# Kernel tuning notes

Measured on AMD Instinct MI355X. Metric: run time of the kernel, lower is better.

Reference implementation:

```python
import jax, jax.numpy as jnp
import numpy as np

BS, X_DIM, KEY_DIM, N_KEYS, TOPK = 16384, 4096, 512, 4096, 16


def setup_inputs() -> dict:
    key = jax.random.key(0)
    k_x, k_keys, k_w, k_b = jax.random.split(key, 4)
    bound = 1.0 / np.sqrt(X_DIM)  # torch Linear default init range
    return {
        "x": jax.random.normal(k_x, (BS, X_DIM), dtype=jnp.float32),
        "keys": jax.random.normal(k_keys, (N_KEYS, KEY_DIM), dtype=jnp.float32),
        "W": jax.random.uniform(k_w, (KEY_DIM, X_DIM), dtype=jnp.float32, minval=-bound, maxval=bound),
        "b": jax.random.uniform(k_b, (KEY_DIM,), dtype=jnp.float32, minval=-bound, maxval=bound),
        "topk": TOPK,
    }


def reference(x, keys, W, b, topk):
    # query = projection(x): [bs, key_dim]
    query = jnp.einsum("bx,kx->bk", x, W) + b
    # scores = query @ keys^T: [bs, n_keys]
    scores = jnp.einsum("bd,nd->bn", query, keys)
    real_topk = min(keys.shape[0], topk)
    topk_scores, topk_idx = jax.lax.top_k(scores, real_topk)  # [bs, k]
    bs = scores.shape[0]
    rows = jnp.arange(bs)[:, None]
    # scatter topk scores into a zero tensor, then softmax over the full row
    gates = jnp.zeros_like(scores).at[rows, topk_idx].set(topk_scores)
    gates = jax.nn.softmax(gates, axis=1)
    return (gates, scores)
```

## Files before the change

kernel.cpp:

```cpp
#include <hip/hip_runtime.h>
#include <stdint.h>

#define BS_T   16384
#define XDIM   4096
#define KDIM   512
#define NKEYS  4096
#define KTOP   16

typedef _Float16 half8  __attribute__((ext_vector_type(8)));
typedef float    floatx4 __attribute__((ext_vector_type(4)));

__device__ static inline void gload_lds16(const void* g, void* l) {
  __builtin_amdgcn_global_load_lds(
      (const __attribute__((address_space(1))) uint32_t*)(uintptr_t)g,
      (__attribute__((address_space(3))) uint32_t*)(uint32_t)(uintptr_t)l,
      16, 0, 0);
}

__global__ __launch_bounds__(256) void cvt_f32_f16_v(const float* __restrict__ in,
                                                     _Float16* __restrict__ out, int n8) {
  int stride = gridDim.x * 256;
  for (int i = blockIdx.x * 256 + threadIdx.x; i < n8; i += stride) {
    float4 v0 = ((const float4*)in)[2 * i];
    float4 v1 = ((const float4*)in)[2 * i + 1];
    half8 h = { (_Float16)v0.x, (_Float16)v0.y, (_Float16)v0.z, (_Float16)v0.w,
                (_Float16)v1.x, (_Float16)v1.y, (_Float16)v1.z, (_Float16)v1.w };
    ((half8*)out)[i] = h;
  }
}

__global__ __launch_bounds__(256, 2)
void gemm1_fused(const float* __restrict__ X, const _Float16* __restrict__ Wh,
                 const float* __restrict__ bias, _Float16* __restrict__ Q) {
  __shared__ __align__(16) _Float16 ldsA[2][64 * 64];
  __shared__ __align__(16) _Float16 ldsB[2][256 * 64];

  const int tid  = threadIdx.x;
  const int lane = tid & 63;
  const int wid  = tid >> 6;
  const int cpx  = gridDim.x >> 3;
  const int bid  = (blockIdx.x & 7) * cpx + (blockIdx.x >> 3);
  const int rowBase = (bid >> 1) * 64;
  const int colBase = (bid & 1) * 256;
  const int wc  = wid * 64;
  const int l15 = lane & 15;
  const int q4  = lane >> 4;
  const int sub   = lane >> 3;
  const int gslot = (lane & 7) ^ sub;

  const int arow  = tid >> 3;
  const int aslot = tid & 7;
  const float* aSrc0 = X + (size_t)(rowBase + arow) * XDIM + aslot * 8;
  const float* aSrc1 = aSrc0 + (size_t)32 * XDIM;
  const int aoff = arow * 128 + ((aslot * 16) ^ ((arow & 7) << 4));
  char* const aD0 = (char*)&ldsA[0][0] + aoff;
  char* const aD1 = (char*)&ldsA[1][0] + aoff;
  const _Float16* const bSrc = Wh + (size_t)(colBase + wc + sub) * XDIM + gslot * 8;
  char* const bD0 = (char*)&ldsB[0][0] + wid * 8192;
  char* const bD1 = (char*)&ldsB[1][0] + wid * 8192;

  floatx4 acc[4][4];
  #pragma unroll
  for (int m = 0; m < 4; ++m)
    #pragma unroll
    for (int n = 0; n < 4; ++n)
      acc[m][n] = (floatx4)0.0f;

  auto stageB = [&](int kt, char* bd) {
    #pragma unroll
    for (int i = 0; i < 8; ++i)
      gload_lds16(bSrc + (size_t)i * 8 * XDIM + kt, bd + i * 1024);
  };
  auto writeA = [&](char* ad, float4 v00, float4 v01, float4 v10, float4 v11) {
    half8 h0 = { (_Float16)v00.x, (_Float16)v00.y, (_Float16)v00.z, (_Float16)v00.w,
                 (_Float16)v01.x, (_Float16)v01.y, (_Float16)v01.z, (_Float16)v01.w };
    half8 h1 = { (_Float16)v10.x, (_Float16)v10.y, (_Float16)v10.z, (_Float16)v10.w,
                 (_Float16)v11.x, (_Float16)v11.y, (_Float16)v11.z, (_Float16)v11.w };
    *(half8*)ad = h0;
    *(half8*)(ad + 4096) = h1;
  };
  auto compute = [&](const char* bA, const char* bB) {
    #pragma unroll
    for (int ks = 0; ks < 2; ++ks) {
      const int s = ks * 4 + q4;
      half8 a[4], b[4];
      #pragma unroll
      for (int m = 0; m < 4; ++m) {
        int row = m * 16 + l15;
        a[m] = *(const half8*)(bA + row * 128 + ((s * 16) ^ ((row & 7) << 4)));
      }
      #pragma unroll
      for (int n = 0; n < 4; ++n) {
        int row = wc + n * 16 + l15;
        b[n] = *(const half8*)(bB + row * 128 + ((s * 16) ^ ((row & 7) << 4)));
      }
      #pragma unroll
      for (int m = 0; m < 4; ++m)
        #pragma unroll
        for (int n = 0; n < 4; ++n)
          acc[m][n] = __builtin_amdgcn_mfma_f32_16x16x32_f16(a[m], b[n], acc[m][n], 0, 0, 0);
    }
  };

  {
    float4 v00 = *(const float4*)(aSrc0);
    float4 v01 = *(const float4*)(aSrc0 + 4);
    float4 v10 = *(const float4*)(aSrc1);
    float4 v11 = *(const float4*)(aSrc1 + 4);
    stageB(0, bD0);
    writeA(aD0, v00, v01, v10, v11);
  }
  __syncthreads();

  #pragma unroll 2
  for (int t = 0; t < 64; ++t) {
    const int pc = t & 1;
    const char* bA = pc ? (const char*)&ldsA[1][0] : (const char*)&ldsA[0][0];
    const char* bB = pc ? (const char*)&ldsB[1][0] : (const char*)&ldsB[0][0];
    char* adN = pc ? aD0 : aD1;
    char* bdN = pc ? bD0 : bD1;

    float4 v00, v01, v10, v11;
    if (t < 63) {
      const int ktn = (t + 1) * 64;
      v00 = *(const float4*)(aSrc0 + ktn);
      v01 = *(const float4*)(aSrc0 + ktn + 4);
      v10 = *(const float4*)(aSrc1 + ktn);
      v11 = *(const float4*)(aSrc1 + ktn + 4);
      stageB(ktn, bdN);
    }
    compute(bA, bB);
    if (t < 63) writeA(adN, v00, v01, v10, v11);
    __syncthreads();
  }

  #pragma unroll
  for (int m = 0; m < 4; ++m) {
    #pragma unroll
    for (int n = 0; n < 4; ++n) {
      int col = colBase + wc + n * 16 + l15;
      float bv = bias[col];
      #pragma unroll
      for (int r = 0; r < 4; ++r) {
        int row = rowBase + m * 16 + q4 * 4 + r;
        Q[(size_t)row * KDIM + col] = (_Float16)(acc[m][n][r] + bv);
      }
    }
  }
}

template<int BM, int BN, int WAVES, int WGN, int MINW>
__global__ __launch_bounds__(WAVES * 64, MINW)
void gemm16(const _Float16* __restrict__ A, const _Float16* __restrict__ B,
            float* __restrict__ outp, int M, int N, int K, int nCol) {
  __shared__ __align__(16) _Float16 ldsA[BM * 64];
  __shared__ __align__(16) _Float16 ldsB[BN * 64];

  const int tid = threadIdx.x;
  const int cpx = gridDim.x >> 3;
  const int bid = (blockIdx.x & 7) * cpx + (blockIdx.x >> 3);
  const int rowBase = (bid / nCol) * BM;
  const int colBase = (bid % nCol) * BN;
  const int lane = tid & 63;
  const int wid  = tid >> 6;
  const int wr = (wid / WGN) * 64;
  const int wc = (wid % WGN) * 64;
  const int l15 = lane & 15;
  const int q4  = lane >> 4;

  const int sub   = lane >> 3;
  const int gslot = (lane & 7) ^ sub;

  constexpr int GROUPS = (BM + BN) / 8;
  constexpr int GPW    = GROUPS / WAVES;

  floatx4 acc[4][4];
  #pragma unroll
  for (int m = 0; m < 4; ++m)
    #pragma unroll
    for (int n = 0; n < 4; ++n)
      acc[m][n] = (floatx4)0.0f;

  for (int kt = 0; kt < K; kt += 64) {
    #pragma unroll
    for (int i = 0; i < GPW; ++i) {
      int g = wid * GPW + i;
      if (g < BM / 8) {
        const _Float16* src = A + (size_t)(rowBase + g * 8 + sub) * K + kt + gslot * 8;
        gload_lds16(src, (char*)ldsA + g * 1024);
      } else {
        int gb = g - BM / 8;
        const _Float16* src = B + (size_t)(colBase + gb * 8 + sub) * K + kt + gslot * 8;
        gload_lds16(src, (char*)ldsB + gb * 1024);
      }
    }
    __syncthreads();

    #pragma unroll
    for (int ks = 0; ks < 2; ++ks) {
      const int s = ks * 4 + q4;
      half8 a[4], b[4];
      #pragma unroll
      for (int m = 0; m < 4; ++m) {
        int row = wr + m * 16 + l15;
        a[m] = *(const half8*)((const char*)ldsA + row * 128 + ((s * 16) ^ ((row & 7) << 4)));
      }
      #pragma unroll
      for (int n = 0; n < 4; ++n) {
        int row = wc + n * 16 + l15;
        b[n] = *(const half8*)((const char*)ldsB + row * 128 + ((s * 16) ^ ((row & 7) << 4)));
      }
      #pragma unroll
      for (int m = 0; m < 4; ++m)
        #pragma unroll
        for (int n = 0; n < 4; ++n)
          acc[m][n] = __builtin_amdgcn_mfma_f32_16x16x32_f16(a[m], b[n], acc[m][n], 0, 0, 0);
    }
    __syncthreads();
  }

  #pragma unroll
  for (int m = 0; m < 4; ++m) {
    #pragma unroll
    for (int n = 0; n < 4; ++n) {
      int col = colBase + wc + n * 16 + l15;
      #pragma unroll
      for (int r = 0; r < 4; ++r) {
        int row = rowBase + wr + m * 16 + q4 * 4 + r;
        outp[(size_t)row * N + col] = acc[m][n][r];
      }
    }
  }
}

__global__ __launch_bounds__(256) void topk_gates_kernel(const float* __restrict__ scores,
                                                         float* __restrict__ gates) {
  __shared__ uint32_t hist[4096];
  __shared__ uint32_t sA[256];
  __shared__ uint32_t av[16], ai[16];
  __shared__ uint32_t sk[KTOP], si[KTOP];
  __shared__ uint32_t cntA, cntC;
  __shared__ int s_p; __shared__ uint32_t s_above;
  __shared__ float gk[KTOP]; __shared__ float s_gother;

  const int tid  = threadIdx.x;
  const int lane = tid & 63;
  const int w    = tid >> 6;
  const float* srow = scores + (size_t)blockIdx.x * NKEYS;

  uint4 z4 = {0, 0, 0, 0};
  #pragma unroll
  for (int i = 0; i < 4; ++i) ((uint4*)hist)[tid + 256 * i] = z4;
  if (tid == 0) { cntA = 0; cntC = 0; }

  uint32_t key[16];
  const int base = (w << 10) + (lane << 4);
  {
    const float4* p4 = (const float4*)(srow + base);
    #pragma unroll
    for (int i = 0; i < 4; ++i) {
      float4 t = p4[i];
      float tv[4] = { t.x, t.y, t.z, t.w };
      #pragma unroll
      for (int c = 0; c < 4; ++c) {
        uint32_t u = __float_as_uint(tv[c]);
        key[i * 4 + c] = u ^ (uint32_t)(((int32_t)u >> 31) | 0x80000000);
      }
    }
  }
  __syncthreads();

  #pragma unroll
  for (int j = 0; j < 16; ++j) atomicAdd(&hist[key[j] >> 20], 1u);
  __syncthreads();

  uint32_t h[16];
  #pragma unroll
  for (int i = 0; i < 16; ++i) h[i] = hist[tid * 16 + i];
  uint32_t sfx[17]; sfx[16] = 0;
  #pragma unroll
  for (int i = 15; i >= 0; --i) sfx[i] = sfx[i + 1] + h[i];
  sA[tid] = sfx[0];
  __syncthreads();
  uint32_t s = sfx[0];
  #pragma unroll
  for (int off = 1; off < 256; off <<= 1) {
    uint32_t add = (tid + off < 256) ? sA[tid + off] : 0;
    __syncthreads();
    s += add; sA[tid] = s;
    __syncthreads();
  }
  const uint32_t exclHi = s - sfx[0];

  #pragma unroll
  for (int i = 0; i < 16; ++i) {
    uint32_t cg = exclHi + sfx[i + 1];
    if (cg < KTOP && cg + h[i] >= KTOP) { s_p = tid * 16 + i; s_above = cg; }
  }
  __syncthreads();
  const uint32_t p = (uint32_t)s_p;
  const uint32_t above = s_above;
  const uint32_t need = KTOP - above;

  uint32_t* ck = hist;
  uint32_t* ci = hist + 2048;
  #pragma unroll
  for (int j = 0; j < 16; ++j) {
    uint32_t b = key[j] >> 20;
    if (b >= p) {
      uint32_t idx = (uint32_t)(base + j);
      if (b > p) { uint32_t pos = atomicAdd(&cntA, 1u); av[pos] = key[j]; ai[pos] = idx; }
      else       { uint32_t pos = atomicAdd(&cntC, 1u); if (pos < 2048u) { ck[pos] = key[j]; ci[pos] = idx; } }
    }
  }
  __syncthreads();

  const uint32_t nA = cntA;
  if (tid < nA) { sk[tid] = av[tid]; si[tid] = ai[tid]; }

  if (w == 0) {
    const uint32_t nC = min(cntC, 2048u);
    for (uint32_t k = 0; k < need; ++k) {
      uint32_t bk = 0, bi = 0xFFFFFFFFu, bp = 0;
      for (uint32_t c = lane; c < nC; c += 64) {
        uint32_t kk = ck[c], ii = ci[c];
        if (kk > bk || (kk == bk && ii < bi)) { bk = kk; bi = ii; bp = c; }
      }
      #pragma unroll
      for (int off = 32; off >= 1; off >>= 1) {
        uint32_t ok = __shfl_down(bk, off);
        uint32_t oi = __shfl_down(bi, off);
        uint32_t op = __shfl_down(bp, off);
        if (ok > bk || (ok == bk && oi < bi)) { bk = ok; bi = oi; bp = op; }
      }
      bp = __shfl(bp, 0);
      if (lane == 0) { ck[bp] = 0; sk[nA + k] = bk; si[nA + k] = bi; }
    }
  }
  __syncthreads();

  if (tid == 0) {
    float f[KTOP]; float mx = 0.f;
    #pragma unroll
    for (int k = 0; k < KTOP; ++k) {
      uint32_t kk = sk[k];
      float fv = (kk & 0x80000000u) ? __uint_as_float(kk ^ 0x80000000u)
                                    : __uint_as_float(~kk);
      f[k] = fv; mx = fmaxf(mx, fv);
    }
    float eo = __expf(-mx);
    float Z = (float)(NKEYS - KTOP) * eo;
    float e[KTOP];
    #pragma unroll
    for (int k = 0; k < KTOP; ++k) { e[k] = __expf(f[k] - mx); Z += e[k]; }
    float inv = 1.f / Z;
    #pragma unroll
    for (int k = 0; k < KTOP; ++k) gk[k] = e[k] * inv;
    s_gother = eo * inv;
  }
  __syncthreads();

  float go = s_gother;
  float4 g4 = { go, go, go, go };
  float* grow = gates + (size_t)blockIdx.x * NKEYS;
  #pragma unroll
  for (int j = 0; j < 4; ++j) ((float4*)grow)[j * 256 + tid] = g4;
  __syncthreads();
  if (tid < KTOP) grow[si[tid]] = gk[tid];
}

extern "C" void kernel_launch(void* const* d_in, const int* in_sizes, int n_in,
                              void* d_out, int out_size, void* d_ws, size_t ws_size,
                              hipStream_t stream) {
  const float* x    = (const float*)d_in[0];
  const float* keys = (const float*)d_in[1];
  const float* W    = (const float*)d_in[2];
  const float* bias = (const float*)d_in[3];
  (void)in_sizes; (void)n_in; (void)out_size; (void)ws_size;

  float* gates  = (float*)d_out;
  float* scores = (float*)d_out + (size_t)BS_T * NKEYS;

  _Float16* W_h = (_Float16*)d_ws;
  _Float16* k_h = W_h + (size_t)KDIM * XDIM;
  _Float16* q_h = k_h + (size_t)NKEYS * KDIM;

  cvt_f32_f16_v<<<dim3(1024), dim3(256), 0, stream>>>(W, W_h, KDIM * XDIM / 8);
  cvt_f32_f16_v<<<dim3(1024), dim3(256), 0, stream>>>(keys, k_h, NKEYS * KDIM / 8);

  gemm1_fused<<<dim3((BS_T / 64) * 2), dim3(256), 0, stream>>>(x, W_h, bias, q_h);

  gemm16<128, 128, 4, 2, 3><<<dim3((BS_T / 128) * (NKEYS / 128)), dim3(256), 0, stream>>>(
      q_h, k_h, scores, BS_T, NKEYS, KDIM, NKEYS / 128);

  topk_gates_kernel<<<dim3(BS_T), dim3(256), 0, stream>>>(scores, gates);
}
```

Baseline: 384.7 us.

## Replace scores GEMM with 256x256 double-buffered pipelined kernel using 8 waves

The generic 128x128 single-buffer scores GEMM is replaced by a specialized 256x256-tile kernel with 512 threads, double-buffered LDS, and prefetch of the next K-tiles interleaved with MFMA phases. It uses explicit vmcnt/lgkmcnt waits, sched barriers, and setprio to overlap global-to-LDS loads with matrix math. The larger tile also raises data reuse per block. LDS use grows to 128KB per block and accumulator registers double, which may limit occupancy.

```diff
diff --git a/kernel.cpp b/kernel.cpp
--- a/kernel.cpp
+++ b/kernel.cpp
@@ -16,6 +16,10 @@
       (__attribute__((address_space(3))) uint32_t*)(uint32_t)(uintptr_t)l,
       16, 0, 0);
 }
+
+#define FULL_BAR() do { __builtin_amdgcn_sched_barrier(0); \
+                        __builtin_amdgcn_s_barrier(); \
+                        __builtin_amdgcn_sched_barrier(0); } while (0)
 
 __global__ __launch_bounds__(256) void cvt_f32_f16_v(const float* __restrict__ in,
                                                      _Float16* __restrict__ out, int n8) {
@@ -149,85 +153,153 @@
   }
 }
 
-template<int BM, int BN, int WAVES, int WGN, int MINW>
-__global__ __launch_bounds__(WAVES * 64, MINW)
-void gemm16(const _Float16* __restrict__ A, const _Float16* __restrict__ B,
-            float* __restrict__ outp, int M, int N, int K, int nCol) {
-  __shared__ __align__(16) _Float16 ldsA[BM * 64];
-  __shared__ __align__(16) _Float16 ldsB[BN * 64];
-
-  const int tid = threadIdx.x;
-  const int cpx = gridDim.x >> 3;
-  const int bid = (blockIdx.x & 7) * cpx + (blockIdx.x >> 3);
-  const int rowBase = (bid / nCol) * BM;
-  const int colBase = (bid % nCol) * BN;
+__global__ __launch_bounds__(512, 2)
+void gemm2_pipe(const _Float16* __restrict__ Aq, const _Float16* __restrict__ Bk,
+                float* __restrict__ outp) {
+  __shared__ __align__(16) _Float16 ldsA[2][256 * 64];
+  __shared__ __align__(16) _Float16 ldsB[2][256 * 64];
+
+  const int tid  = threadIdx.x;
   const int lane = tid & 63;
   const int wid  = tid >> 6;
-  const int wr = (wid / WGN) * 64;
-  const int wc = (wid % WGN) * 64;
+  const int cpx  = gridDim.x >> 3;
+  const int bid  = (blockIdx.x & 7) * cpx + (blockIdx.x >> 3);
+  const int nCol = NKEYS / 256;
+  const int rowBase = (bid / nCol) * 256;
+  const int colBase = (bid % nCol) * 256;
+  const int wm = wid >> 2;
+  const int wn = wid & 3;
   const int l15 = lane & 15;
   const int q4  = lane >> 4;
-
   const int sub   = lane >> 3;
   const int gslot = (lane & 7) ^ sub;
 
-  constexpr int GROUPS = (BM + BN) / 8;
-  constexpr int GPW    = GROUPS / WAVES;
-
-  floatx4 acc[4][4];
-  #pragma unroll
-  for (int m = 0; m < 4; ++m)
+  const _Float16* aSrc = Aq + (size_t)rowBase * KDIM;
+  const _Float16* bSrc = Bk + (size_t)colBase * KDIM;
+
+  auto stageHalf = [&](const _Float16* src, char* ldsbase, int kt, int h) {
+    #pragma unroll
+    for (int j = 0; j < 2; ++j) {
+      int g = h * 16 + wid * 2 + j;
+      gload_lds16(src + (size_t)(g * 8 + sub) * KDIM + kt + gslot * 8,
+                  ldsbase + g * 1024);
+    }
+  };
+  auto ld8 = [&](const char* base, int row, int s) {
+    return *(const half8*)(base + row * 128 + ((s * 16) ^ ((row & 7) << 4)));
+  };
+
+  floatx4 acc[8][4];
+  #pragma unroll
+  for (int m = 0; m < 8; ++m)
     #pragma unroll
     for (int n = 0; n < 4; ++n)
       acc[m][n] = (floatx4)0.0f;
 
-  for (int kt = 0; kt < K; kt += 64) {
-    #pragma unroll
-    for (int i = 0; i < GPW; ++i) {
-      int g = wid * GPW + i;
-      if (g < BM / 8) {
-        const _Float16* src = A + (size_t)(rowBase + g * 8 + sub) * K + kt + gslot * 8;
-        gload_lds16(src, (char*)ldsA + g * 1024);
-      } else {
-        int gb = g - BM / 8;
-        const _Float16* src = B + (size_t)(colBase + gb * 8 + sub) * K + kt + gslot * 8;
-        gload_lds16(src, (char*)ldsB + gb * 1024);
-      }
-    }
-    __syncthreads();
-
-    #pragma unroll
-    for (int ks = 0; ks < 2; ++ks) {
-      const int s = ks * 4 + q4;
-      half8 a[4], b[4];
-      #pragma unroll
-      for (int m = 0; m < 4; ++m) {
-        int row = wr + m * 16 + l15;
-        a[m] = *(const half8*)((const char*)ldsA + row * 128 + ((s * 16) ^ ((row & 7) << 4)));
-      }
-      #pragma unroll
-      for (int n = 0; n < 4; ++n) {
-        int row = wc + n * 16 + l15;
-        b[n] = *(const half8*)((const char*)ldsB + row * 128 + ((s * 16) ^ ((row & 7) << 4)));
-      }
-      #pragma unroll
-      for (int m = 0; m < 4; ++m)
+  stageHalf(aSrc, (char*)ldsA[0], 0, 0);
+  stageHalf(aSrc, (char*)ldsA[0], 0, 1);
+  stageHalf(bSrc, (char*)ldsB[0], 0, 0);
+  stageHalf(bSrc, (char*)ldsB[0], 0, 1);
+  stageHalf(aSrc, (char*)ldsA[1], 64, 0);
+  stageHalf(aSrc, (char*)ldsA[1], 64, 1);
+  stageHalf(bSrc, (char*)ldsB[1], 64, 0);
+  stageHalf(bSrc, (char*)ldsB[1], 64, 1);
+  asm volatile("s_waitcnt vmcnt(8)" ::: "memory");
+  FULL_BAR();
+
+  for (int t = 0; t < 8; ++t) {
+    const char* bA = (const char*)ldsA[t & 1];
+    const char* bB = (const char*)ldsB[t & 1];
+    char* sA = (char*)ldsA[t & 1];
+    char* sB = (char*)ldsB[t & 1];
+    const int ktn = (t + 2) * 64;
+    const bool st = (t < 6);
+
+    half8 a[4][2], b[4][2];
+
+    #pragma unroll
+    for (int m = 0; m < 4; ++m)
+      #pragma unroll
+      for (int kk = 0; kk < 2; ++kk)
+        a[m][kk] = ld8(bA, wm * 128 + m * 16 + l15, kk * 4 + q4);
+    #pragma unroll
+    for (int n = 0; n < 4; ++n)
+      #pragma unroll
+      for (int kk = 0; kk < 2; ++kk)
+        b[n][kk] = ld8(bB, wn * 64 + n * 16 + l15, kk * 4 + q4);
+    FULL_BAR();
+    asm volatile("s_waitcnt lgkmcnt(0)" ::: "memory");
+    __builtin_amdgcn_sched_barrier(0);
+    __builtin_amdgcn_s_setprio(1);
+    #pragma unroll
+    for (int m = 0; m < 4; ++m)
+      #pragma unroll
+      for (int n = 0; n < 2; ++n)
         #pragma unroll
-        for (int n = 0; n < 4; ++n)
-          acc[m][n] = __builtin_amdgcn_mfma_f32_16x16x32_f16(a[m], b[n], acc[m][n], 0, 0, 0);
-    }
-    __syncthreads();
-  }
-
-  #pragma unroll
-  for (int m = 0; m < 4; ++m) {
+        for (int kk = 0; kk < 2; ++kk)
+          acc[m][n] = __builtin_amdgcn_mfma_f32_16x16x32_f16(a[m][kk], b[n][kk], acc[m][n], 0, 0, 0);
+    __builtin_amdgcn_s_setprio(0);
+    FULL_BAR();
+
+    if (st) stageHalf(bSrc, sB, ktn, 0);
+    __builtin_amdgcn_sched_barrier(0);
+    __builtin_amdgcn_s_setprio(1);
+    #pragma unroll
+    for (int m = 0; m < 4; ++m)
+      #pragma unroll
+      for (int n = 2; n < 4; ++n)
+        #pragma unroll
+        for (int kk = 0; kk < 2; ++kk)
+          acc[m][n] = __builtin_amdgcn_mfma_f32_16x16x32_f16(a[m][kk], b[n][kk], acc[m][n], 0, 0, 0);
+    __builtin_amdgcn_s_setprio(0);
+    FULL_BAR();
+
+    #pragma unroll
+    for (int m = 0; m < 4; ++m)
+      #pragma unroll
+      for (int kk = 0; kk < 2; ++kk)
+        a[m][kk] = ld8(bA, wm * 128 + (m + 4) * 16 + l15, kk * 4 + q4);
+    if (st) stageHalf(bSrc, sB, ktn, 1);
+    FULL_BAR();
+    asm volatile("s_waitcnt lgkmcnt(0)" ::: "memory");
+    __builtin_amdgcn_sched_barrier(0);
+    __builtin_amdgcn_s_setprio(1);
+    #pragma unroll
+    for (int m = 0; m < 4; ++m)
+      #pragma unroll
+      for (int n = 0; n < 2; ++n)
+        #pragma unroll
+        for (int kk = 0; kk < 2; ++kk)
+          acc[m + 4][n] = __builtin_amdgcn_mfma_f32_16x16x32_f16(a[m][kk], b[n][kk], acc[m + 4][n], 0, 0, 0);
+    __builtin_amdgcn_s_setprio(0);
+    FULL_BAR();
+
+    if (st) { stageHalf(aSrc, sA, ktn, 0); stageHalf(aSrc, sA, ktn, 1); }
+    __builtin_amdgcn_sched_barrier(0);
+    __builtin_amdgcn_s_setprio(1);
+    #pragma unroll
+    for (int m = 0; m < 4; ++m)
+      #pragma unroll
+      for (int n = 2; n < 4; ++n)
+        #pragma unroll
+        for (int kk = 0; kk < 2; ++kk)
+          acc[m + 4][n] = __builtin_amdgcn_mfma_f32_16x16x32_f16(a[m][kk], b[n][kk], acc[m + 4][n], 0, 0, 0);
+    __builtin_amdgcn_s_setprio(0);
+    __builtin_amdgcn_sched_barrier(0);
+    if (t < 6)      asm volatile("s_waitcnt vmcnt(8)" ::: "memory");
+    else if (t == 6) asm volatile("s_waitcnt vmcnt(0)" ::: "memory");
+    FULL_BAR();
+  }
+
+  #pragma unroll
+  for (int m = 0; m < 8; ++m) {
     #pragma unroll
     for (int n = 0; n < 4; ++n) {
-      int col = colBase + wc + n * 16 + l15;
+      int col = colBase + wn * 64 + n * 16 + l15;
       #pragma unroll
       for (int r = 0; r < 4; ++r) {
-        int row = rowBase + wr + m * 16 + q4 * 4 + r;
-        outp[(size_t)row * N + col] = acc[m][n][r];
+        int row = rowBase + wm * 128 + m * 16 + q4 * 4 + r;
+        outp[(size_t)row * NKEYS + col] = acc[m][n][r];
       }
     }
   }
@@ -390,8 +462,8 @@
 
   gemm1_fused<<<dim3((BS_T / 64) * 2), dim3(256), 0, stream>>>(x, W_h, bias, q_h);
 
-  gemm16<128, 128, 4, 2, 3><<<dim3((BS_T / 128) * (NKEYS / 128)), dim3(256), 0, stream>>>(
-      q_h, k_h, scores, BS_T, NKEYS, KDIM, NKEYS / 128);
+  gemm2_pipe<<<dim3((BS_T / 256) * (NKEYS / 256)), dim3(512), 0, stream>>>(
+      q_h, k_h, scores);
 
   topk_gates_kernel<<<dim3(BS_T), dim3(256), 0, stream>>>(scores, gates);
 }
```

Result: faster. 359.9 us (-6.5%).
